# Kernel optimization log

Measured on AMD Instinct MI355X. Metric: run time of the kernel, lower is better.

## Reference

```python
import jax, jax.numpy as jnp
import numpy as np

V, D, L, H, T_BLK, DFF = 50257, 768, 12, 12, 1024, 4096
DK = D // H
LN_EPS = 1e-5


def setup_inputs() -> dict:
    key = jax.random.key(0)
    ks = jax.random.split(key, 16)
    s = 0.02
    inp = {
        "idx": jax.random.randint(ks[0], (2, 1024), 0, V),
        "tok_emb": jax.random.normal(ks[1], (V, D), jnp.float32) * s,
        "pos_emb": jax.random.normal(ks[2], (1, T_BLK, D), jnp.float32) * s,
        "ln1_w": jnp.ones((L, D), jnp.float32),
        "ln1_b": jnp.zeros((L, D), jnp.float32),
        "qkv_w": jax.random.normal(ks[3], (L, 3 * D, D), jnp.float32) * s,
        "qkv_b": jnp.zeros((L, 3 * D), jnp.float32),
        "proj_w": jax.random.normal(ks[4], (L, D, D), jnp.float32) * s,
        "proj_b": jnp.zeros((L, D), jnp.float32),
        "ln2_w": jnp.ones((L, D), jnp.float32),
        "ln2_b": jnp.zeros((L, D), jnp.float32),
        "ff1_w": jax.random.normal(ks[5], (L, DFF, D), jnp.float32) * s,
        "ff1_b": jnp.zeros((L, DFF), jnp.float32),
        "ff2_w": jax.random.normal(ks[6], (L, D, DFF), jnp.float32) * s,
        "ff2_b": jnp.zeros((L, D), jnp.float32),
        "lnf_w": jnp.ones((D,), jnp.float32),
        "lnf_b": jnp.zeros((D,), jnp.float32),
        "head_w": jax.random.normal(ks[7], (V, D), jnp.float32) * s,
    }
    return inp


def _layernorm(x, w, b):
    mu = jnp.mean(x, axis=-1, keepdims=True)
    var = jnp.var(x, axis=-1, keepdims=True)
    return (x - mu) * jax.lax.rsqrt(var + LN_EPS) * w + b


def _gpt_forward(idx, tok_emb, pos_emb, ln1_w, ln1_b, qkv_w, qkv_b, proj_w, proj_b,
                 ln2_w, ln2_b, ff1_w, ff1_b, ff2_w, ff2_b, lnf_w, lnf_b, head_w):
    B, T = idx.shape
    x = tok_emb[idx] + pos_emb[:, :T, :]  # [B,T,D]
    mask = jnp.tril(jnp.ones((T, T), bool))  # causal
    scale = 1.0 / np.sqrt(DK)

    def step(x, p):
        l1w, l1b, qw, qb, pw, pb, l2w, l2b, f1w, f1b, f2w, f2b = p
        h = _layernorm(x, l1w, l1b)
        qkv = h @ qw.T + qb  # [B,T,3D]
        q, k, v = jnp.split(qkv, 3, axis=-1)
        q = q.reshape(B, T, H, DK).transpose(0, 2, 1, 3)  # [B,H,T,DK]
        k = k.reshape(B, T, H, DK).transpose(0, 2, 1, 3)
        v = v.reshape(B, T, H, DK).transpose(0, 2, 1, 3)
        att = jnp.einsum('bhtd,bhsd->bhts', q, k) * scale
        att = jnp.where(mask, att, -jnp.inf)
        att = jax.nn.softmax(att, axis=-1)
        y = jnp.einsum('bhts,bhsd->bhtd', att, v)
        y = y.transpose(0, 2, 1, 3).reshape(B, T, D)
        x = x + y @ pw.T + pb
        h2 = _layernorm(x, l2w, l2b)
        ff = jax.nn.gelu(h2 @ f1w.T + f1b, approximate=False) @ f2w.T + f2b
        return x + ff, None

    params = (ln1_w, ln1_b, qkv_w, qkv_b, proj_w, proj_b,
              ln2_w, ln2_b, ff1_w, ff1_b, ff2_w, ff2_b)
    x, _ = jax.lax.scan(step, x, params)
    x = _layernorm(x, lnf_w, lnf_b)
    return x @ head_w.T  # [B,T,V] logits


def reference(idx, tok_emb, pos_emb, ln1_w, ln1_b, qkv_w, qkv_b, proj_w, proj_b,
              ln2_w, ln2_b, ff1_w, ff1_b, ff2_w, ff2_b, lnf_w, lnf_b, head_w):
    return _gpt_forward(idx, tok_emb, pos_emb, ln1_w, ln1_b, qkv_w, qkv_b, proj_w,
                        proj_b, ln2_w, ln2_b, ff1_w, ff1_b, ff2_w, ff2_b,
                        lnf_w, lnf_b, head_w)
```

## Files before the change

kernel.cpp:

```cpp
#include <hip/hip_runtime.h>
#include <hip/hip_bf16.h>
#include <math.h>

#define Dm 768
#define Tt 1024
#define Bb 2
#define Hh 12
#define DFF 4096
#define Ll 12
#define Vv 50257
#define ROWS (Bb*Tt)
#define LN_EPS 1e-5f

typedef unsigned int uint;
typedef unsigned short ushort;
typedef float f32x4 __attribute__((ext_vector_type(4)));
typedef short bf16x8 __attribute__((ext_vector_type(8)));
typedef ushort us8 __attribute__((ext_vector_type(8)));

__device__ __forceinline__ ushort f2bf(float f) {
  uint u = __builtin_bit_cast(uint, f);
  u += 0x7FFFu + ((u >> 16) & 1u);
  return (ushort)(u >> 16);
}

#define GLL(gp, lp)                                                          \
  __builtin_amdgcn_global_load_lds(                                          \
      (const __attribute__((address_space(1))) uint*)(gp),                   \
      (__attribute__((address_space(3))) uint*)(lp), 16, 0, 0)

__global__ __launch_bounds__(256) void embed_kernel(
    const int* __restrict__ idx, const float* __restrict__ tok,
    const float* __restrict__ pos, float* __restrict__ x) {
  const int row = blockIdx.x;
  const int t = row & (Tt - 1);
  const float* tsrc = tok + (size_t)idx[row] * Dm;
  const float* psrc = pos + (size_t)t * Dm;
  float* dst = x + (size_t)row * Dm;
  for (int i = threadIdx.x; i < Dm; i += 256) dst[i] = tsrc[i] + psrc[i];
}

__global__ __launch_bounds__(256) void ln_kernel(
    const float* __restrict__ x, const float* __restrict__ w,
    const float* __restrict__ b, ushort* __restrict__ out) {
  const int row = blockIdx.x;
  const int tid = threadIdx.x;
  const float* src = x + (size_t)row * Dm;
  float v[3];
  float sum = 0.f, sq = 0.f;
#pragma unroll
  for (int i = 0; i < 3; i++) {
    v[i] = src[tid + i * 256];
    sum += v[i]; sq += v[i] * v[i];
  }
#pragma unroll
  for (int off = 32; off > 0; off >>= 1) {
    sum += __shfl_xor(sum, off);
    sq  += __shfl_xor(sq, off);
  }
  __shared__ float red[8];
  const int wid = tid >> 6, lane = tid & 63;
  if (lane == 0) { red[wid] = sum; red[wid + 4] = sq; }
  __syncthreads();
  sum = red[0] + red[1] + red[2] + red[3];
  sq  = red[4] + red[5] + red[6] + red[7];
  const float mu = sum * (1.f / Dm);
  const float var = sq * (1.f / Dm) - mu * mu;
  const float rstd = rsqrtf(var + LN_EPS);
  ushort* dst = out + (size_t)row * Dm;
#pragma unroll
  for (int i = 0; i < 3; i++) {
    const int d = tid + i * 256;
    dst[d] = f2bf((v[i] - mu) * rstd * w[d] + b[d]);
  }
}

__global__ __launch_bounds__(256) void red_ln(
    const float* __restrict__ part, int nsk, const float* __restrict__ bias,
    float* __restrict__ x, const float* __restrict__ w,
    const float* __restrict__ b, ushort* __restrict__ out) {
  const int row = blockIdx.x;
  const int tid = threadIdx.x;
  float v[3];
  float sum = 0.f, sq = 0.f;
#pragma unroll
  for (int i = 0; i < 3; i++) {
    const int d = tid + i * 256;
    const size_t off = (size_t)row * Dm + d;
    float s = x[off] + bias[d];
    for (int k = 0; k < nsk; k++) s += part[(size_t)k * ROWS * Dm + off];
    x[off] = s;
    v[i] = s;
    sum += s; sq += s * s;
  }
#pragma unroll
  for (int off = 32; off > 0; off >>= 1) {
    sum += __shfl_xor(sum, off);
    sq  += __shfl_xor(sq, off);
  }
  __shared__ float red[8];
  const int wid = tid >> 6, lane = tid & 63;
  if (lane == 0) { red[wid] = sum; red[wid + 4] = sq; }
  __syncthreads();
  sum = red[0] + red[1] + red[2] + red[3];
  sq  = red[4] + red[5] + red[6] + red[7];
  const float mu = sum * (1.f / Dm);
  const float var = sq * (1.f / Dm) - mu * mu;
  const float rstd = rsqrtf(var + LN_EPS);
  ushort* dst = out + (size_t)row * Dm;
#pragma unroll
  for (int i = 0; i < 3; i++) {
    const int d = tid + i * 256;
    dst[d] = f2bf((v[i] - mu) * rstd * w[d] + b[d]);
  }
}

__global__ __launch_bounds__(256) void convert_w(
    const float* __restrict__ s, ushort* __restrict__ d, int n4) {
  const int stride = gridDim.x * 256;
  for (int i = blockIdx.x * 256 + threadIdx.x; i < n4; i += stride) {
    const float4 v = ((const float4*)s)[i];
    ushort4 o;
    o.x = f2bf(v.x); o.y = f2bf(v.y); o.z = f2bf(v.z); o.w = f2bf(v.w);
    ((ushort4*)d)[i] = o;
  }
}

__global__ __launch_bounds__(256) void convert_w4(
    const float* __restrict__ s0, const float* __restrict__ s1,
    const float* __restrict__ s2, const float* __restrict__ s3,
    ushort* __restrict__ d, int c0, int c1, int c2, int c3) {
  const int total = c0 + c1 + c2 + c3;
  const int stride = gridDim.x * 256;
  for (int i = blockIdx.x * 256 + threadIdx.x; i < total; i += stride) {
    int j = i; const float* s;
    if (j < c0) s = s0;
    else if ((j -= c0) < c1) s = s1;
    else if ((j -= c1) < c2) s = s2;
    else { j -= c2; s = s3; }
    const float4 v = ((const float4*)s)[j];
    ushort4 o;
    o.x = f2bf(v.x); o.y = f2bf(v.y); o.z = f2bf(v.z); o.w = f2bf(v.w);
    ((ushort4*)d)[i] = o;
  }
}

#define EPI_QKV 0
#define EPI_PART 1
#define EPI_BIAS_GELU 2
#define EPI_NONE 3

template <int EPI>
__global__ __launch_bounds__(256) void gemm_mfma(
    const ushort* __restrict__ A, const ushort* __restrict__ B,
    const float* __restrict__ bias, void* __restrict__ Cv,
    int Kloop, int Kstr, int Nloc, int ldC) {
  __shared__ char lds[32768];
  const int tid = threadIdx.x;
  const int l = tid & 63;
  const int wid = __builtin_amdgcn_readfirstlane(tid >> 6);
  const int wr = wid >> 1, wc = wid & 1;
  const int m0 = blockIdx.y * 128;
  const int n0 = blockIdx.x * 128;
  const int z = (EPI == EPI_PART) ? blockIdx.z : 0;
  if (EPI == EPI_PART) { A += (size_t)z * Kloop; B += (size_t)z * Kloop; }

  const int cperm = (((l & 3) ^ ((l >> 3) & 3)) * 8);
  const ushort* gA = A + (size_t)(m0 + wid * 32 + (l >> 2)) * Kstr + cperm;
  int rB = n0 + wid * 32 + (l >> 2);
  rB = min(rB, Nloc - 1);
  const ushort* gB = B + (size_t)rB * Kstr + cperm;

  const int rdSw = (l & 15) * 64 + (((l >> 4) ^ ((l >> 1) & 3)) * 16);
  const int aRd = wr * 4096 + rdSw;
  const int bRd = 8192 + wc * 4096 + rdSw;

  f32x4 acc[4][4] = {};
  const int nt = Kloop / 32;

  {
    const int lb = wid * 2048;
    GLL(gA, lds + lb);          GLL(gA + 16 * Kstr, lds + lb + 1024);
    GLL(gB, lds + 8192 + lb);   GLL(gB + 16 * Kstr, lds + 8192 + lb + 1024);
  }

  for (int t = 0; t < nt; ++t) {
    __syncthreads();
    if (t + 1 < nt) {
      const int base = ((t + 1) & 1) * 16384;
      const int lb = base + wid * 2048;
      const ushort* a = gA + (t + 1) * 32;
      const ushort* b = gB + (t + 1) * 32;
      GLL(a, lds + lb);         GLL(a + 16 * Kstr, lds + lb + 1024);
      GLL(b, lds + 8192 + lb);  GLL(b + 16 * Kstr, lds + 8192 + lb + 1024);
    }
    const int base = (t & 1) * 16384;
    bf16x8 av[4], bv[4];
#pragma unroll
    for (int i = 0; i < 4; ++i) {
      av[i] = *(const bf16x8*)(lds + base + aRd + i * 1024);
      bv[i] = *(const bf16x8*)(lds + base + bRd + i * 1024);
    }
#pragma unroll
    for (int i = 0; i < 4; ++i)
#pragma unroll
      for (int j = 0; j < 4; ++j)
        acc[i][j] = __builtin_amdgcn_mfma_f32_16x16x32_bf16(
            av[i], bv[j], acc[i][j], 0, 0, 0);
  }

#pragma unroll
  for (int fm = 0; fm < 4; ++fm) {
    const int row0 = m0 + wr * 64 + fm * 16 + (l >> 4) * 4;
#pragma unroll
    for (int fn = 0; fn < 4; ++fn) {
      const int col = n0 + wc * 64 + fn * 16 + (l & 15);
      if (col >= Nloc) continue;
      float bi = 0.f;
      if (EPI == EPI_QKV || EPI == EPI_BIAS_GELU) bi = bias[col];
#pragma unroll
      for (int r = 0; r < 4; ++r) {
        float v = acc[fm][fn][r] + bi;
        const size_t off = (size_t)(row0 + r) * ldC + col;
        if (EPI == EPI_BIAS_GELU) {
          v = 0.5f * v * (1.f + erff(v * 0.70710678118654752f));
          ((ushort*)Cv)[off] = f2bf(v);
        } else if (EPI == EPI_QKV) {
          ((ushort*)Cv)[off] = f2bf(v);
        } else if (EPI == EPI_PART) {
          ((float*)Cv)[(size_t)z * ROWS * ldC + off] = v;
        } else {
          ((float*)Cv)[off] = v;
        }
      }
    }
  }
}

__global__ __launch_bounds__(256) void transpose_v(
    const ushort* __restrict__ qkv, ushort* __restrict__ vTg) {
  __shared__ ushort tile[64][65];
  const int tc = blockIdx.x, bh = blockIdx.y;
  const int b = bh / Hh, h = bh - b * Hh;
  const int tid = threadIdx.x;
#pragma unroll
  for (int i = 0; i < 2; i++) {
    const int c = tid + i * 256;
    const int t = c >> 3, d0 = (c & 7) * 8;
    us8 v = *(const us8*)(qkv + (size_t)(b * Tt + tc * 64 + t) * 2304 +
                          2 * Dm + h * 64 + d0);
#pragma unroll
    for (int j = 0; j < 8; j++) tile[t][d0 + j] = v[j];
  }
  __syncthreads();
#pragma unroll
  for (int i = 0; i < 2; i++) {
    const int c = tid + i * 256;
    const int d = c >> 3, t0 = (c & 7) * 8;
    us8 o;
#pragma unroll
    for (int j = 0; j < 8; j++) o[j] = tile[t0 + j][d];
    *(us8*)(vTg + (size_t)(bh * 64 + d) * Tt + tc * 64 + t0) = o;
  }
}

__global__ __launch_bounds__(128) void attn_mfma(
    const ushort* __restrict__ qkv, const ushort* __restrict__ vTg,
    ushort* __restrict__ y) {
  __shared__ char lds[36864];
  const int tid = threadIdx.x;
  const int l = tid & 63;
  const int w = tid >> 6;
  const int s = l & 15, g = l >> 4;
  const int bq = blockIdx.x, h = blockIdx.y, b = blockIdx.z;
  const int bh = b * Hh + h;

  const int qrow = bq * 32 + w * 16 + s;
  const ushort* qp = qkv + (size_t)(b * Tt + qrow) * 2304 + h * 64 + g * 8;
  const bf16x8 aq0 = *(const bf16x8*)qp;
  const bf16x8 aq1 = *(const bf16x8*)(qp + 32);

  size_t gofs[8];
#pragma unroll
  for (int i = 0; i < 8; i++) {
    const int c = tid + i * 128;
    if (i < 4) {
      const int kr = c >> 3;
      gofs[i] = (size_t)(b * Tt + kr) * 2304 + Dm + h * 64 + ((c & 7) ^ (kr & 7)) * 8;
    } else {
      const int cv = c - 512;
      const int vr = cv >> 3;
      gofs[i] = (size_t)(bh * 64 + vr) * Tt + ((cv & 7) ^ (vr & 7)) * 8;
    }
  }

#define ASTAGE(kt, base)                                                     \
  do {                                                                       \
    _Pragma("unroll")                                                        \
    for (int i = 0; i < 8; i++) {                                            \
      const ushort* p = (i < 4) ? (qkv + gofs[i] + (size_t)(kt) * 147456)    \
                                : (vTg + gofs[i] + (kt) * 64);               \
      GLL(p, lds + (base) + tid * 16 + i * 2048);                            \
    }                                                                        \
  } while (0)

  f32x4 oc[4] = {};
  float mrun[4], lrun[4];
#pragma unroll
  for (int r = 0; r < 4; r++) { mrun[r] = -INFINITY; lrun[r] = 0.f; }

  const int pB = 32768 + w * 2048;
  const int kSw = (s & 7);
  const int nkt = (bq >> 1) + 1;

  ASTAGE(0, 0);
  for (int kt = 0; kt < nkt; ++kt) {
    __syncthreads();
    if (kt + 1 < nkt) ASTAGE(kt + 1, ((kt + 1) & 1) * 16384);
    const int cur = (kt & 1) * 16384;

    f32x4 sc[4];
#pragma unroll
    for (int jn = 0; jn < 4; jn++) {
      const int krow = cur + (jn * 16 + s) * 128;
      const bf16x8 bk0 = *(const bf16x8*)(lds + krow + ((g ^ kSw) * 16));
      const bf16x8 bk1 = *(const bf16x8*)(lds + krow + (((4 + g) ^ kSw) * 16));
      f32x4 z = {};
      z = __builtin_amdgcn_mfma_f32_16x16x32_bf16(aq0, bk0, z, 0, 0, 0);
      z = __builtin_amdgcn_mfma_f32_16x16x32_bf16(aq1, bk1, z, 0, 0, 0);
      sc[jn] = z;
    }

    float cr[4];
    const bool diag = (kt == nkt - 1);
#pragma unroll
    for (int r = 0; r < 4; r++) {
      const int rowg = bq * 32 + w * 16 + g * 4 + r;
      float v[4];
#pragma unroll
      for (int jn = 0; jn < 4; jn++) {
        v[jn] = sc[jn][r] * 0.125f;
        if (diag && (kt * 64 + jn * 16 + s) > rowg) v[jn] = -INFINITY;
      }
      float mx = fmaxf(fmaxf(v[0], v[1]), fmaxf(v[2], v[3]));
      mx = fmaxf(mx, __shfl_xor(mx, 1));
      mx = fmaxf(mx, __shfl_xor(mx, 2));
      mx = fmaxf(mx, __shfl_xor(mx, 4));
      mx = fmaxf(mx, __shfl_xor(mx, 8));
      const float mnew = fmaxf(mrun[r], mx);
      const float corr = __expf(mrun[r] - mnew);
      mrun[r] = mnew;
      float ps = 0.f;
#pragma unroll
      for (int jn = 0; jn < 4; jn++) {
        const float p = __expf(v[jn] - mnew);
        ps += p;
        *(ushort*)(lds + pB + (g * 4 + r) * 128 +
                   (((2 * jn + (s >> 3)) ^ g) * 16) + (s & 7) * 2) = f2bf(p);
      }
      ps += __shfl_xor(ps, 1);
      ps += __shfl_xor(ps, 2);
      ps += __shfl_xor(ps, 4);
      ps += __shfl_xor(ps, 8);
      lrun[r] = lrun[r] * corr + ps;
      cr[r] = corr;
    }

    const float c01 = (s & 1) ? cr[1] : cr[0];
    const float c23 = (s & 1) ? cr[3] : cr[2];
    const float csel = (s & 2) ? c23 : c01;
    const float ccol = __shfl(csel, ((s >> 2) << 4) | s);
#pragma unroll
    for (int fm = 0; fm < 4; fm++) {
      oc[fm][0] *= ccol; oc[fm][1] *= ccol;
      oc[fm][2] *= ccol; oc[fm][3] *= ccol;
    }

    const bf16x8 bp0 = *(const bf16x8*)(lds + pB + s * 128 + ((g ^ (s >> 2)) * 16));
    const bf16x8 bp1 = *(const bf16x8*)(lds + pB + s * 128 + (((4 + g) ^ (s >> 2)) * 16));
#pragma unroll
    for (int fm = 0; fm < 4; fm++) {
      const int vrow = cur + 8192 + (fm * 16 + s) * 128;
      const bf16x8 av0 = *(const bf16x8*)(lds + vrow + ((g ^ kSw) * 16));
      const bf16x8 av1 = *(const bf16x8*)(lds + vrow + (((4 + g) ^ kSw) * 16));
      oc[fm] = __builtin_amdgcn_mfma_f32_16x16x32_bf16(av0, bp0, oc[fm], 0, 0, 0);
      oc[fm] = __builtin_amdgcn_mfma_f32_16x16x32_bf16(av1, bp1, oc[fm], 0, 0, 0);
    }
  }

  float li[4];
#pragma unroll
  for (int r = 0; r < 4; r++) li[r] = 1.f / lrun[r];
  const float l01 = (s & 1) ? li[1] : li[0];
  const float l23 = (s & 1) ? li[3] : li[2];
  const float lsel = (s & 2) ? l23 : l01;
  const float lcol = __shfl(lsel, ((s >> 2) << 4) | s);
  ushort* yp = y + (size_t)(b * Tt + qrow) * Dm + h * 64;
#pragma unroll
  for (int fm = 0; fm < 4; fm++) {
    ushort4 o4;
    o4.x = f2bf(oc[fm][0] * lcol);
    o4.y = f2bf(oc[fm][1] * lcol);
    o4.z = f2bf(oc[fm][2] * lcol);
    o4.w = f2bf(oc[fm][3] * lcol);
    *(ushort4*)(yp + fm * 16 + g * 4) = o4;
  }
}

extern "C" void kernel_launch(void* const* d_in, const int* in_sizes, int n_in,
                              void* d_out, int out_size, void* d_ws, size_t ws_size,
                              hipStream_t stream) {
  const int* idx = (const int*)d_in[0];
  const float* tok = (const float*)d_in[1];
  const float* pos = (const float*)d_in[2];
  const float* ln1w = (const float*)d_in[3];
  const float* ln1b = (const float*)d_in[4];
  const float* qkvw = (const float*)d_in[5];
  const float* qkvb = (const float*)d_in[6];
  const float* projw = (const float*)d_in[7];
  const float* projb = (const float*)d_in[8];
  const float* ln2w = (const float*)d_in[9];
  const float* ln2b = (const float*)d_in[10];
  const float* ff1w = (const float*)d_in[11];
  const float* ff1b = (const float*)d_in[12];
  const float* ff2w = (const float*)d_in[13];
  const float* ff2b = (const float*)d_in[14];
  const float* lnfw = (const float*)d_in[15];
  const float* lnfb = (const float*)d_in[16];
  const float* headw = (const float*)d_in[17];
  float* out = (float*)d_out;

  char* ws = (char*)d_ws;
  ushort* h    = (ushort*)ws;
  float*  x    = (float*)(ws + 3145728);
  ushort* y    = (ushort*)(ws + 9437184);
  ushort* qkv  = (ushort*)(ws + 12582912);
  ushort* vTg  = (ushort*)(ws + 22020096);
  ushort* ff   = (ushort*)(ws + 25165824);
  ushort* wb   = (ushort*)(ws + 41943040);
  ushort* hb   = (ushort*)(ws + 3145728);
  float* projPart = (float*)(ws + 12582912);
  float* ff2Part  = (float*)(ws + 9437184);

  const int oProj = 3 * Dm * Dm;
  const int oFF1  = oProj + Dm * Dm;
  const int oFF2  = oFF1 + DFF * Dm;

  embed_kernel<<<ROWS, 256, 0, stream>>>(idx, tok, pos, x);
  ln_kernel<<<ROWS, 256, 0, stream>>>(x, ln1w, ln1b, h);

  for (int l = 0; l < Ll; l++) {
    convert_w4<<<2048, 256, 0, stream>>>(
        qkvw + (size_t)l * 3 * Dm * Dm, projw + (size_t)l * Dm * Dm,
        ff1w + (size_t)l * DFF * Dm, ff2w + (size_t)l * Dm * DFF, wb,
        3 * Dm * Dm / 4, Dm * Dm / 4, DFF * Dm / 4, Dm * DFF / 4);
    gemm_mfma<EPI_QKV><<<dim3(18, 16), 256, 0, stream>>>(
        h, wb, qkvb + l * 3 * Dm, qkv, Dm, Dm, 3 * Dm, 3 * Dm);
    transpose_v<<<dim3(16, 24), 256, 0, stream>>>(qkv, vTg);
    attn_mfma<<<dim3(32, Hh, Bb), 128, 0, stream>>>(qkv, vTg, y);
    gemm_mfma<EPI_PART><<<dim3(6, 16, 2), 256, 0, stream>>>(
        y, wb + oProj, nullptr, projPart, Dm / 2, Dm, Dm, Dm);
    red_ln<<<ROWS, 256, 0, stream>>>(projPart, 2, projb + l * Dm, x,
                                     ln2w + l * Dm, ln2b + l * Dm, h);
    gemm_mfma<EPI_BIAS_GELU><<<dim3(32, 16), 256, 0, stream>>>(
        h, wb + oFF1, ff1b + l * DFF, ff, Dm, Dm, DFF, DFF);
    gemm_mfma<EPI_PART><<<dim3(6, 16, 2), 256, 0, stream>>>(
        ff, wb + oFF2, nullptr, ff2Part, DFF / 2, DFF, Dm, Dm);
    const float* nw = (l == Ll - 1) ? lnfw : ln1w + (l + 1) * Dm;
    const float* nb = (l == Ll - 1) ? lnfb : ln1b + (l + 1) * Dm;
    red_ln<<<ROWS, 256, 0, stream>>>(ff2Part, 2, ff2b + l * Dm, x, nw, nb, h);
  }

  const int ch0 = 25088;
  const int ch1 = Vv - ch0;
  convert_w<<<2048, 256, 0, stream>>>(headw, hb, ch0 * (Dm / 4));
  gemm_mfma<EPI_NONE><<<dim3(ch0 / 128, 16), 256, 0, stream>>>(
      h, hb, nullptr, out, Dm, Dm, ch0, Vv);
  convert_w<<<2048, 256, 0, stream>>>(headw + (size_t)ch0 * Dm, hb, ch1 * (Dm / 4));
  gemm_mfma<EPI_NONE><<<dim3((ch1 + 127) / 128, 16), 256, 0, stream>>>(
      h, hb, nullptr, out + ch0, Dm, Dm, ch1, Vv);
}
```

Before: 2.146 ms.

## Convert all weights to bf16 in one upfront kernel and swizzle GEMM tiles across XCDs

All layer weights and the head weight are now converted to bf16 by a single kernel at the start into a larger persistent workspace, replacing the per-layer conversion launches and the two chunked head conversions. The head GEMM becomes a single launch over the full vocabulary. The GEMM kernel also remaps block ids so consecutive tiles on each XCD share N panels, aiming for better L2 reuse. In exchange the workspace grows substantially, and the total fp32 read and bf16 write traffic is unchanged, so the gain comes from fewer launches and better parallelism rather than less conversion work.

```diff
diff --git a/kernel.cpp b/kernel.cpp
--- a/kernel.cpp
+++ b/kernel.cpp
@@ -115,33 +115,50 @@
   }
 }
 
-__global__ __launch_bounds__(256) void convert_w(
-    const float* __restrict__ s, ushort* __restrict__ d, int n4) {
+#define LW4 2162688
+#define SQ4 5308416
+#define SP4 1769472
+#define SF4 9437184
+#define SH4 9649344
+#define CUM1 (SQ4)
+#define CUM2 (SQ4+SP4)
+#define CUM3 (SQ4+SP4+SF4)
+#define CUM4 (SQ4+SP4+2*SF4)
+#define N4ALL (SQ4+SP4+2*SF4+SH4)
+#define HEADB4 25952256
+
+__global__ __launch_bounds__(256) void convert_gpt(
+    const float* __restrict__ qkvw, const float* __restrict__ projw,
+    const float* __restrict__ ff1w, const float* __restrict__ ff2w,
+    const float* __restrict__ headw, ushort* __restrict__ wb) {
   const int stride = gridDim.x * 256;
-  for (int i = blockIdx.x * 256 + threadIdx.x; i < n4; i += stride) {
-    const float4 v = ((const float4*)s)[i];
-    ushort4 o;
-    o.x = f2bf(v.x); o.y = f2bf(v.y); o.z = f2bf(v.z); o.w = f2bf(v.w);
-    ((ushort4*)d)[i] = o;
-  }
-}
-
-__global__ __launch_bounds__(256) void convert_w4(
-    const float* __restrict__ s0, const float* __restrict__ s1,
-    const float* __restrict__ s2, const float* __restrict__ s3,
-    ushort* __restrict__ d, int c0, int c1, int c2, int c3) {
-  const int total = c0 + c1 + c2 + c3;
-  const int stride = gridDim.x * 256;
-  for (int i = blockIdx.x * 256 + threadIdx.x; i < total; i += stride) {
-    int j = i; const float* s;
-    if (j < c0) s = s0;
-    else if ((j -= c0) < c1) s = s1;
-    else if ((j -= c1) < c2) s = s2;
-    else { j -= c2; s = s3; }
-    const float4 v = ((const float4*)s)[j];
-    ushort4 o;
-    o.x = f2bf(v.x); o.y = f2bf(v.y); o.z = f2bf(v.z); o.w = f2bf(v.w);
-    ((ushort4*)d)[i] = o;
+  for (int i = blockIdx.x * 256 + threadIdx.x; i < N4ALL; i += stride) {
+    const float* s; size_t d4;
+    if (i < CUM1) {
+      const int j = i, l = j / 442368, o = j - l * 442368;
+      s = qkvw + (size_t)j * 4;
+      d4 = (size_t)l * LW4 + o;
+    } else if (i < CUM2) {
+      const int j = i - CUM1, l = j / 147456, o = j - l * 147456;
+      s = projw + (size_t)j * 4;
+      d4 = (size_t)l * LW4 + 442368 + o;
+    } else if (i < CUM3) {
+      const int j = i - CUM2, l = j / 786432, o = j - l * 786432;
+      s = ff1w + (size_t)j * 4;
+      d4 = (size_t)l * LW4 + 589824 + o;
+    } else if (i < CUM4) {
+      const int j = i - CUM3, l = j / 786432, o = j - l * 786432;
+      s = ff2w + (size_t)j * 4;
+      d4 = (size_t)l * LW4 + 1376256 + o;
+    } else {
+      const int j = i - CUM4;
+      s = headw + (size_t)j * 4;
+      d4 = (size_t)HEADB4 + j;
+    }
+    const float4 v = *(const float4*)s;
+    ushort4 o4;
+    o4.x = f2bf(v.x); o4.y = f2bf(v.y); o4.z = f2bf(v.z); o4.w = f2bf(v.w);
+    ((ushort4*)wb)[d4] = o4;
   }
 }
 
@@ -160,8 +177,17 @@
   const int l = tid & 63;
   const int wid = __builtin_amdgcn_readfirstlane(tid >> 6);
   const int wr = wid >> 1, wc = wid & 1;
-  const int m0 = blockIdx.y * 128;
-  const int n0 = blockIdx.x * 128;
+
+  const int nbx = gridDim.x, nby = gridDim.y;
+  const int nwg = nbx * nby;
+  const int bid = blockIdx.y * nbx + blockIdx.x;
+  const int xcd = bid & 7, loc = bid >> 3;
+  const int q8 = nwg >> 3, r8 = nwg & 7;
+  const int swz = (xcd < r8 ? xcd * (q8 + 1) : r8 * (q8 + 1) + (xcd - r8) * q8) + loc;
+  const int pan = swz / nby, mrw = swz - pan * nby;
+  const int m0 = mrw * 128;
+  const int n0 = pan * 128;
+
   const int z = (EPI == EPI_PART) ? blockIdx.z : 0;
   if (EPI == EPI_PART) { A += (size_t)z * Kloop; B += (size_t)z * Kloop; }
 
@@ -438,45 +464,38 @@
   ushort* vTg  = (ushort*)(ws + 22020096);
   ushort* ff   = (ushort*)(ws + 25165824);
   ushort* wb   = (ushort*)(ws + 41943040);
-  ushort* hb   = (ushort*)(ws + 3145728);
   float* projPart = (float*)(ws + 12582912);
   float* ff2Part  = (float*)(ws + 9437184);
 
   const int oProj = 3 * Dm * Dm;
   const int oFF1  = oProj + Dm * Dm;
   const int oFF2  = oFF1 + DFF * Dm;
-
+  const size_t LWE = 8650752;
+  ushort* headwb = wb + (size_t)HEADB4 * 4;
+
+  convert_gpt<<<4096, 256, 0, stream>>>(qkvw, projw, ff1w, ff2w, headw, wb);
   embed_kernel<<<ROWS, 256, 0, stream>>>(idx, tok, pos, x);
   ln_kernel<<<ROWS, 256, 0, stream>>>(x, ln1w, ln1b, h);
 
   for (int l = 0; l < Ll; l++) {
-    convert_w4<<<2048, 256, 0, stream>>>(
-        qkvw + (size_t)l * 3 * Dm * Dm, projw + (size_t)l * Dm * Dm,
-        ff1w + (size_t)l * DFF * Dm, ff2w + (size_t)l * Dm * DFF, wb,
-        3 * Dm * Dm / 4, Dm * Dm / 4, DFF * Dm / 4, Dm * DFF / 4);
+    ushort* wl = wb + (size_t)l * LWE;
     gemm_mfma<EPI_QKV><<<dim3(18, 16), 256, 0, stream>>>(
-        h, wb, qkvb + l * 3 * Dm, qkv, Dm, Dm, 3 * Dm, 3 * Dm);
+        h, wl, qkvb + l * 3 * Dm, qkv, Dm, Dm, 3 * Dm, 3 * Dm);
     transpose_v<<<dim3(16, 24), 256, 0, stream>>>(qkv, vTg);
     attn_mfma<<<dim3(32, Hh, Bb), 128, 0, stream>>>(qkv, vTg, y);
     gemm_mfma<EPI_PART><<<dim3(6, 16, 2), 256, 0, stream>>>(
-        y, wb + oProj, nullptr, projPart, Dm / 2, Dm, Dm, Dm);
+        y, wl + oProj, nullptr, projPart, Dm / 2, Dm, Dm, Dm);
     red_ln<<<ROWS, 256, 0, stream>>>(projPart, 2, projb + l * Dm, x,
                                      ln2w + l * Dm, ln2b + l * Dm, h);
     gemm_mfma<EPI_BIAS_GELU><<<dim3(32, 16), 256, 0, stream>>>(
-        h, wb + oFF1, ff1b + l * DFF, ff, Dm, Dm, DFF, DFF);
+        h, wl + oFF1, ff1b + l * DFF, ff, Dm, Dm, DFF, DFF);
     gemm_mfma<EPI_PART><<<dim3(6, 16, 2), 256, 0, stream>>>(
-        ff, wb + oFF2, nullptr, ff2Part, DFF / 2, DFF, Dm, Dm);
+        ff, wl + oFF2, nullptr, ff2Part, DFF / 2, DFF, Dm, Dm);
     const float* nw = (l == Ll - 1) ? lnfw : ln1w + (l + 1) * Dm;
     const float* nb = (l == Ll - 1) ? lnfb : ln1b + (l + 1) * Dm;
     red_ln<<<ROWS, 256, 0, stream>>>(ff2Part, 2, ff2b + l * Dm, x, nw, nb, h);
   }
 
-  const int ch0 = 25088;
-  const int ch1 = Vv - ch0;
-  convert_w<<<2048, 256, 0, stream>>>(headw, hb, ch0 * (Dm / 4));
-  gemm_mfma<EPI_NONE><<<dim3(ch0 / 128, 16), 256, 0, stream>>>(
-      h, hb, nullptr, out, Dm, Dm, ch0, Vv);
-  convert_w<<<2048, 256, 0, stream>>>(headw + (size_t)ch0 * Dm, hb, ch1 * (Dm / 4));
-  gemm_mfma<EPI_NONE><<<dim3((ch1 + 127) / 128, 16), 256, 0, stream>>>(
-      h, hb, nullptr, out + ch0, Dm, Dm, ch1, Vv);
-}
+  gemm_mfma<EPI_NONE><<<dim3(393, 16), 256, 0, stream>>>(
+      h, headwb, nullptr, out, Dm, Dm, Vv, Vv);
+}
```

Result: slower. 2.325 ms (+8.4%).

## Convert all weights upfront, fuse V transpose into QKV epilogue, merge embed+LN

Applied to the files above, without the earlier changes.

All layer and head weights are now converted to bf16 once, up front, into one large workspace region instead of per layer. The V-transpose kernel is removed; the QKV GEMM epilogue writes V columns directly in transposed [b,h,d,t] layout. The embedding add is fused with the first layernorm, and the head GEMM becomes a single launch over all vocab columns. This cuts launch count and redundant passes over the activations. The cost is a much larger bf16 weight buffer in the workspace, plus scattered 8-byte stores in the QKV epilogue.

```diff
diff --git a/kernel.cpp b/kernel.cpp
--- a/kernel.cpp
+++ b/kernel.cpp
@@ -29,28 +29,23 @@
       (const __attribute__((address_space(1))) uint*)(gp),                   \
       (__attribute__((address_space(3))) uint*)(lp), 16, 0, 0)
 
-__global__ __launch_bounds__(256) void embed_kernel(
+__global__ __launch_bounds__(256) void embed_ln(
     const int* __restrict__ idx, const float* __restrict__ tok,
-    const float* __restrict__ pos, float* __restrict__ x) {
+    const float* __restrict__ pos, const float* __restrict__ w,
+    const float* __restrict__ b, float* __restrict__ x,
+    ushort* __restrict__ out) {
   const int row = blockIdx.x;
   const int t = row & (Tt - 1);
+  const int tid = threadIdx.x;
   const float* tsrc = tok + (size_t)idx[row] * Dm;
   const float* psrc = pos + (size_t)t * Dm;
-  float* dst = x + (size_t)row * Dm;
-  for (int i = threadIdx.x; i < Dm; i += 256) dst[i] = tsrc[i] + psrc[i];
-}
-
-__global__ __launch_bounds__(256) void ln_kernel(
-    const float* __restrict__ x, const float* __restrict__ w,
-    const float* __restrict__ b, ushort* __restrict__ out) {
-  const int row = blockIdx.x;
-  const int tid = threadIdx.x;
-  const float* src = x + (size_t)row * Dm;
   float v[3];
   float sum = 0.f, sq = 0.f;
 #pragma unroll
   for (int i = 0; i < 3; i++) {
-    v[i] = src[tid + i * 256];
+    const int d = tid + i * 256;
+    v[i] = tsrc[d] + psrc[d];
+    x[(size_t)row * Dm + d] = v[i];
     sum += v[i]; sq += v[i] * v[i];
   }
 #pragma unroll
@@ -126,25 +121,6 @@
   }
 }
 
-__global__ __launch_bounds__(256) void convert_w4(
-    const float* __restrict__ s0, const float* __restrict__ s1,
-    const float* __restrict__ s2, const float* __restrict__ s3,
-    ushort* __restrict__ d, int c0, int c1, int c2, int c3) {
-  const int total = c0 + c1 + c2 + c3;
-  const int stride = gridDim.x * 256;
-  for (int i = blockIdx.x * 256 + threadIdx.x; i < total; i += stride) {
-    int j = i; const float* s;
-    if (j < c0) s = s0;
-    else if ((j -= c0) < c1) s = s1;
-    else if ((j -= c1) < c2) s = s2;
-    else { j -= c2; s = s3; }
-    const float4 v = ((const float4*)s)[j];
-    ushort4 o;
-    o.x = f2bf(v.x); o.y = f2bf(v.y); o.z = f2bf(v.z); o.w = f2bf(v.w);
-    ((ushort4*)d)[i] = o;
-  }
-}
-
 #define EPI_QKV 0
 #define EPI_PART 1
 #define EPI_BIAS_GELU 2
@@ -154,7 +130,7 @@
 __global__ __launch_bounds__(256) void gemm_mfma(
     const ushort* __restrict__ A, const ushort* __restrict__ B,
     const float* __restrict__ bias, void* __restrict__ Cv,
-    int Kloop, int Kstr, int Nloc, int ldC) {
+    void* __restrict__ Cv2, int Kloop, int Kstr, int Nloc, int ldC) {
   __shared__ char lds[32768];
   const int tid = threadIdx.x;
   const int l = tid & 63;
@@ -218,6 +194,18 @@
       if (col >= Nloc) continue;
       float bi = 0.f;
       if (EPI == EPI_QKV || EPI == EPI_BIAS_GELU) bi = bias[col];
+      if (EPI == EPI_QKV && col >= 2 * Dm) {
+        const int hh = (col - 2 * Dm) >> 6, dd = col & 63;
+        const int bI = row0 >> 10, t0 = row0 & (Tt - 1);
+        ushort4 o4;
+        o4.x = f2bf(acc[fm][fn][0] + bi);
+        o4.y = f2bf(acc[fm][fn][1] + bi);
+        o4.z = f2bf(acc[fm][fn][2] + bi);
+        o4.w = f2bf(acc[fm][fn][3] + bi);
+        *(ushort4*)((ushort*)Cv2 +
+                    ((size_t)((bI * Hh + hh) * 64 + dd)) * Tt + t0) = o4;
+        continue;
+      }
 #pragma unroll
       for (int r = 0; r < 4; ++r) {
         float v = acc[fm][fn][r] + bi;
@@ -234,33 +222,6 @@
         }
       }
     }
-  }
-}
-
-__global__ __launch_bounds__(256) void transpose_v(
-    const ushort* __restrict__ qkv, ushort* __restrict__ vTg) {
-  __shared__ ushort tile[64][65];
-  const int tc = blockIdx.x, bh = blockIdx.y;
-  const int b = bh / Hh, h = bh - b * Hh;
-  const int tid = threadIdx.x;
-#pragma unroll
-  for (int i = 0; i < 2; i++) {
-    const int c = tid + i * 256;
-    const int t = c >> 3, d0 = (c & 7) * 8;
-    us8 v = *(const us8*)(qkv + (size_t)(b * Tt + tc * 64 + t) * 2304 +
-                          2 * Dm + h * 64 + d0);
-#pragma unroll
-    for (int j = 0; j < 8; j++) tile[t][d0 + j] = v[j];
-  }
-  __syncthreads();
-#pragma unroll
-  for (int i = 0; i < 2; i++) {
-    const int c = tid + i * 256;
-    const int d = c >> 3, t0 = (c & 7) * 8;
-    us8 o;
-#pragma unroll
-    for (int j = 0; j < 8; j++) o[j] = tile[t0 + j][d];
-    *(us8*)(vTg + (size_t)(bh * 64 + d) * Tt + tc * 64 + t0) = o;
   }
 }
 
@@ -438,45 +399,43 @@
   ushort* vTg  = (ushort*)(ws + 22020096);
   ushort* ff   = (ushort*)(ws + 25165824);
   ushort* wb   = (ushort*)(ws + 41943040);
-  ushort* hb   = (ushort*)(ws + 3145728);
   float* projPart = (float*)(ws + 12582912);
   float* ff2Part  = (float*)(ws + 9437184);
 
-  const int oProj = 3 * Dm * Dm;
-  const int oFF1  = oProj + Dm * Dm;
-  const int oFF2  = oFF1 + DFF * Dm;
-
-  embed_kernel<<<ROWS, 256, 0, stream>>>(idx, tok, pos, x);
-  ln_kernel<<<ROWS, 256, 0, stream>>>(x, ln1w, ln1b, h);
+  const size_t oPROJ = (size_t)Ll * 3 * Dm * Dm;
+  const size_t oFF1  = oPROJ + (size_t)Ll * Dm * Dm;
+  const size_t oFF2  = oFF1 + (size_t)Ll * DFF * Dm;
+  const size_t oHEAD = oFF2 + (size_t)Ll * Dm * DFF;
+
+  convert_w<<<2048, 256, 0, stream>>>(qkvw, wb, (int)(oPROJ / 4));
+  convert_w<<<2048, 256, 0, stream>>>(projw, wb + oPROJ, (int)((oFF1 - oPROJ) / 4));
+  convert_w<<<2048, 256, 0, stream>>>(ff1w, wb + oFF1, (int)((oFF2 - oFF1) / 4));
+  convert_w<<<2048, 256, 0, stream>>>(ff2w, wb + oFF2, (int)((oHEAD - oFF2) / 4));
+  convert_w<<<2048, 256, 0, stream>>>(headw, wb + oHEAD, (int)((size_t)Vv * Dm / 4));
+
+  embed_ln<<<ROWS, 256, 0, stream>>>(idx, tok, pos, ln1w, ln1b, x, h);
 
   for (int l = 0; l < Ll; l++) {
-    convert_w4<<<2048, 256, 0, stream>>>(
-        qkvw + (size_t)l * 3 * Dm * Dm, projw + (size_t)l * Dm * Dm,
-        ff1w + (size_t)l * DFF * Dm, ff2w + (size_t)l * Dm * DFF, wb,
-        3 * Dm * Dm / 4, Dm * Dm / 4, DFF * Dm / 4, Dm * DFF / 4);
     gemm_mfma<EPI_QKV><<<dim3(18, 16), 256, 0, stream>>>(
-        h, wb, qkvb + l * 3 * Dm, qkv, Dm, Dm, 3 * Dm, 3 * Dm);
-    transpose_v<<<dim3(16, 24), 256, 0, stream>>>(qkv, vTg);
+        h, wb + (size_t)l * 3 * Dm * Dm, qkvb + l * 3 * Dm, qkv, vTg,
+        Dm, Dm, 3 * Dm, 3 * Dm);
     attn_mfma<<<dim3(32, Hh, Bb), 128, 0, stream>>>(qkv, vTg, y);
     gemm_mfma<EPI_PART><<<dim3(6, 16, 2), 256, 0, stream>>>(
-        y, wb + oProj, nullptr, projPart, Dm / 2, Dm, Dm, Dm);
+        y, wb + oPROJ + (size_t)l * Dm * Dm, nullptr, projPart, nullptr,
+        Dm / 2, Dm, Dm, Dm);
     red_ln<<<ROWS, 256, 0, stream>>>(projPart, 2, projb + l * Dm, x,
                                      ln2w + l * Dm, ln2b + l * Dm, h);
     gemm_mfma<EPI_BIAS_GELU><<<dim3(32, 16), 256, 0, stream>>>(
-        h, wb + oFF1, ff1b + l * DFF, ff, Dm, Dm, DFF, DFF);
+        h, wb + oFF1 + (size_t)l * DFF * Dm, ff1b + l * DFF, ff, nullptr,
+        Dm, Dm, DFF, DFF);
     gemm_mfma<EPI_PART><<<dim3(6, 16, 2), 256, 0, stream>>>(
-        ff, wb + oFF2, nullptr, ff2Part, DFF / 2, DFF, Dm, Dm);
+        ff, wb + oFF2 + (size_t)l * Dm * DFF, nullptr, ff2Part, nullptr,
+        DFF / 2, DFF, Dm, Dm);
     const float* nw = (l == Ll - 1) ? lnfw : ln1w + (l + 1) * Dm;
     const float* nb = (l == Ll - 1) ? lnfb : ln1b + (l + 1) * Dm;
     red_ln<<<ROWS, 256, 0, stream>>>(ff2Part, 2, ff2b + l * Dm, x, nw, nb, h);
   }
 
-  const int ch0 = 25088;
-  const int ch1 = Vv - ch0;
-  convert_w<<<2048, 256, 0, stream>>>(headw, hb, ch0 * (Dm / 4));
-  gemm_mfma<EPI_NONE><<<dim3(ch0 / 128, 16), 256, 0, stream>>>(
-      h, hb, nullptr, out, Dm, Dm, ch0, Vv);
-  convert_w<<<2048, 256, 0, stream>>>(headw + (size_t)ch0 * Dm, hb, ch1 * (Dm / 4));
-  gemm_mfma<EPI_NONE><<<dim3((ch1 + 127) / 128, 16), 256, 0, stream>>>(
-      h, hb, nullptr, out + ch0, Dm, Dm, ch1, Vv);
-}
+  gemm_mfma<EPI_NONE><<<dim3(393, 16), 256, 0, stream>>>(
+      h, wb + oHEAD, nullptr, out, nullptr, Dm, Dm, Vv, Vv);
+}
```

After: 2.245 ms. 1.05x slower.
